# Kernel tuning notes

Hardware: AMD Instinct MI355X
Metric: run time of the kernel (lower is better)

The kernel has to match this reference:

```python
import jax, jax.numpy as jnp
import numpy as np

EMBED = 512
MLP_DIM = 2048
B, T = 4, 4096
EPS = 1e-5


def setup_inputs() -> dict:
    key = jax.random.key(0)
    ks = jax.random.split(key, 8)
    s = lambda fan_in: 1.0 / np.sqrt(fan_in)
    inp = {
        "x": jax.random.normal(ks[0], (B, T, EMBED), dtype=jnp.float32),
        "Wq": jax.random.uniform(ks[1], (EMBED, EMBED), jnp.float32, -s(EMBED), s(EMBED)),
        "bq": jnp.zeros((EMBED,), jnp.float32),
        "Wk": jax.random.uniform(ks[2], (EMBED, EMBED), jnp.float32, -s(EMBED), s(EMBED)),
        "bk": jnp.zeros((EMBED,), jnp.float32),
        "Wv": jax.random.uniform(ks[3], (EMBED, EMBED), jnp.float32, -s(EMBED), s(EMBED)),
        "bv": jnp.zeros((EMBED,), jnp.float32),
        "W1": jax.random.uniform(ks[4], (EMBED, MLP_DIM), jnp.float32, -s(EMBED), s(EMBED)),
        "b1": jnp.zeros((MLP_DIM,), jnp.float32),
        "W2": jax.random.uniform(ks[5], (MLP_DIM, EMBED), jnp.float32, -s(MLP_DIM), s(MLP_DIM)),
        "b2": jnp.zeros((EMBED,), jnp.float32),
        "ln1_g": jnp.ones((EMBED,), jnp.float32),
        "ln1_b": jnp.zeros((EMBED,), jnp.float32),
        "ln2_g": jnp.ones((EMBED,), jnp.float32),
        "ln2_b": jnp.zeros((EMBED,), jnp.float32),
    }
    return inp


def _layernorm(x, g, b):
    mu = x.mean(-1, keepdims=True)
    var = ((x - mu) ** 2).mean(-1, keepdims=True)
    return (x - mu) * jax.lax.rsqrt(var + EPS) * g + b


def reference(x, Wq, bq, Wk, bk, Wv, bv, W1, b1, W2, b2, ln1_g, ln1_b, ln2_g, ln2_b):
    # pre-LN causal self-attention (single head)
    h = _layernorm(x, ln1_g, ln1_b)
    q = h @ Wq + bq  # [B,T,D]
    k = h @ Wk + bk
    v = h @ Wv + bv
    scale = 1.0 / jnp.sqrt(jnp.float32(EMBED))
    scores = jnp.einsum("btd,bsd->bts", q, k) * scale  # [B,T,T]
    mask = jnp.tril(jnp.ones((T, T), dtype=bool))
    scores = jnp.where(mask, scores, -jnp.inf)
    # NOTE: source applies softmax over the ENTIRE [T,T] matrix per batch
    # element (global max + global sum), not per-row. Replicate exactly.
    m = scores.max(axis=(-2, -1), keepdims=True)
    e = jnp.exp(scores - m)
    attn = e / e.sum(axis=(-2, -1), keepdims=True)
    x = x + jnp.einsum("bts,bsd->btd", attn, v)
    # MLP
    h2 = _layernorm(x, ln2_g, ln2_b)
    x = x + (jax.nn.gelu(h2 @ W1 + b1, approximate=False) @ W2 + b2)
    return x
```

## Files before the change

### kernel.cpp

```cpp
#include <hip/hip_runtime.h>
#include <hip/hip_bf16.h>
#include <math.h>

#define EMBED 512
#define MLPD  2048
#define NB    4
#define TS    4096
#define BT    (NB*TS)
#define BK    64
#define NTILES_TRI 528

typedef __attribute__((ext_vector_type(4))) float f32x4;
typedef __attribute__((ext_vector_type(8))) short s16x8;
typedef __hip_bfloat16 bf16_t;

__device__ __forceinline__ void gload16(const void* g, void* l) {
  __builtin_amdgcn_global_load_lds(
      (const __attribute__((address_space(1))) void*)g,
      (__attribute__((address_space(3))) void*)l, 16, 0, 0);
}

__device__ __forceinline__ float fast_erf(float y) {
  const float ay = fabsf(y);
  const float t = __builtin_amdgcn_rcpf(1.0f + 0.3275911f*ay);
  float poly = 1.061405429f;
  poly = poly*t - 1.453152027f;
  poly = poly*t + 1.421413741f;
  poly = poly*t - 0.284496736f;
  poly = poly*t + 0.254829592f;
  poly = poly*t;
  const float e = 1.0f - poly*__expf(-ay*ay);
  return copysignf(e, y);
}


__device__ __forceinline__ void gemm_core(
    const bf16_t* __restrict__ A, int lda,
    const bf16_t* __restrict__ Bt, int ldb,
    int kmax, bf16_t* Alds, bf16_t* Blds, f32x4 acc[4][4])
{
  const int tid = threadIdx.x;
  const int w  = tid >> 6;
  const int l  = tid & 63;
  const int wr = w >> 1, wc = w & 1;
  const int fr = l & 15, fg = l >> 4;

  #pragma unroll
  for (int i = 0; i < 4; ++i)
    #pragma unroll
    for (int j = 0; j < 4; ++j)
      #pragma unroll
      for (int e = 0; e < 4; ++e)
        acc[i][j][e] = 0.0f;

  const int srow = w*32 + (l >> 3);
  const int sx = (((l & 7) ^ ((l >> 3) & 7)))*8;
  const int rsw = fr & 7;

  for (int k0 = 0; k0 < kmax; k0 += BK) {
    __syncthreads();
    #pragma unroll
    for (int c = 0; c < 4; ++c) {
      const bf16_t* ga = A  + (size_t)(srow + c*8)*lda + (k0 + sx);
      const bf16_t* gb = Bt + (size_t)(srow + c*8)*ldb + (k0 + sx);
      gload16(ga, Alds + (w*32 + c*8)*BK);
      gload16(gb, Blds + (w*32 + c*8)*BK);
    }
    __syncthreads();
    #pragma unroll
    for (int kk = 0; kk < BK; kk += 32) {
      s16x8 av[4], bv[4];
      const int ch = (kk >> 3) + fg;
      const int co = (ch ^ rsw) << 3;
      #pragma unroll
      for (int mf = 0; mf < 4; ++mf)
        av[mf] = *(const s16x8*)(Alds + (wr*64 + mf*16 + fr)*BK + co);
      #pragma unroll
      for (int nf = 0; nf < 4; ++nf)
        bv[nf] = *(const s16x8*)(Blds + (wc*64 + nf*16 + fr)*BK + co);
      #pragma unroll
      for (int mf = 0; mf < 4; ++mf)
        #pragma unroll
        for (int nf = 0; nf < 4; ++nf)
          acc[mf][nf] = __builtin_amdgcn_mfma_f32_16x16x32_bf16(
              av[mf], bv[nf], acc[mf][nf], 0, 0, 0);
    }
  }
}

__device__ __forceinline__ void gemm_core_deep(
    const bf16_t* __restrict__ A, int lda,
    const bf16_t* __restrict__ Bt, int ldb,
    int kmax, bf16_t* Alds, bf16_t* Blds, f32x4 acc[4][4])
{
  const int tid = threadIdx.x;
  const int w  = tid >> 6;
  const int l  = tid & 63;
  const int wr = w >> 1, wc = w & 1;
  const int fr = l & 15, fg = l >> 4;

  #pragma unroll
  for (int i = 0; i < 4; ++i)
    #pragma unroll
    for (int j = 0; j < 4; ++j)
      #pragma unroll
      for (int e = 0; e < 4; ++e)
        acc[i][j][e] = 0.0f;

  const int srow = w*32 + (l >> 3);
  const int sx = (((l & 7) ^ ((l >> 3) & 7)))*8;
  const int rsw = fr & 7;
  const int T = kmax >> 6;

  #define ISSUE_A(t_) do { \
    bf16_t* dst = Alds + ((t_) % 3)*(128*BK); \
    const int k0_ = (t_)*BK; \
    _Pragma("unroll") \
    for (int c = 0; c < 4; ++c) \
      gload16(A + (size_t)(srow + c*8)*lda + (k0_ + sx), dst + (w*32 + c*8)*BK); \
  } while (0)
  #define ISSUE_B(t_) do { \
    bf16_t* dst = Blds + ((t_) & 1)*(128*BK); \
    const int k0_ = (t_)*BK; \
    _Pragma("unroll") \
    for (int c = 0; c < 4; ++c) \
      gload16(Bt + (size_t)(srow + c*8)*ldb + (k0_ + sx), dst + (w*32 + c*8)*BK); \
  } while (0)

  ISSUE_A(0); ISSUE_B(0);
  if (T > 1) ISSUE_A(1);

  for (int t = 0; t < T; ++t) {
    if (t <= T - 3) {
      ISSUE_B(t + 1); ISSUE_A(t + 2);
      asm volatile("s_waitcnt vmcnt(12)" ::: "memory");
    } else if (t == T - 2) {
      ISSUE_B(t + 1);
      asm volatile("s_waitcnt vmcnt(8)" ::: "memory");
    } else {
      asm volatile("s_waitcnt vmcnt(0)" ::: "memory");
    }
    __builtin_amdgcn_s_barrier();
    bf16_t* Ac = Alds + (t % 3)*(128*BK);
    bf16_t* Bc = Blds + (t & 1)*(128*BK);
    #pragma unroll
    for (int kk = 0; kk < BK; kk += 32) {
      s16x8 av[4], bv[4];
      const int ch = (kk >> 3) + fg;
      const int co = (ch ^ rsw) << 3;
      #pragma unroll
      for (int mf = 0; mf < 4; ++mf)
        av[mf] = *(const s16x8*)(Ac + (wr*64 + mf*16 + fr)*BK + co);
      #pragma unroll
      for (int nf = 0; nf < 4; ++nf)
        bv[nf] = *(const s16x8*)(Bc + (wc*64 + nf*16 + fr)*BK + co);
      #pragma unroll
      for (int mf = 0; mf < 4; ++mf)
        #pragma unroll
        for (int nf = 0; nf < 4; ++nf)
          acc[mf][nf] = __builtin_amdgcn_mfma_f32_16x16x32_bf16(
              av[mf], bv[nf], acc[mf][nf], 0, 0, 0);
    }
    __builtin_amdgcn_s_barrier();
  }
  #undef ISSUE_A
  #undef ISSUE_B
}

#define EPILOGUE_SETUP \
  const int l = threadIdx.x & 63; const int w = threadIdx.x >> 6; \
  const int wr = w >> 1, wc = w & 1, fr = l & 15, fg = l >> 4;

__global__ void __launch_bounds__(256) k_proj_qkv(
    const bf16_t* __restrict__ A,
    const bf16_t* __restrict__ wqt, const bf16_t* __restrict__ wkt,
    const bf16_t* __restrict__ wvt,
    const float* __restrict__ bq, const float* __restrict__ bk,
    const float* __restrict__ bv,
    bf16_t* __restrict__ qb, bf16_t* __restrict__ kb, bf16_t* __restrict__ vt)
{
  __shared__ __align__(16) bf16_t Alds[128*BK];
  __shared__ __align__(16) bf16_t Blds[128*BK];
  f32x4 acc[4][4];
  const int z = blockIdx.z;
  const bf16_t* Wt = (z == 0) ? wqt : (z == 1) ? wkt : wvt;
  const float* bias = (z == 0) ? bq : (z == 1) ? bk : bv;
  const int bx = blockIdx.x;
  const int m0 = ((bx & 7)*16 + (bx >> 3))*128;
  const int n0 = blockIdx.y*128;
  gemm_core(A + (size_t)m0*EMBED, EMBED, Wt + (size_t)n0*EMBED, EMBED, EMBED,
            Alds, Blds, acc);
  EPILOGUE_SETUP
  if (z < 2) {
    bf16_t* outp = (z == 0) ? qb : kb;
    #pragma unroll
    for (int mf = 0; mf < 4; ++mf)
      #pragma unroll
      for (int nf = 0; nf < 4; ++nf) {
        const int col = n0 + wc*64 + nf*16 + fr;
        const float bb = bias[col];
        #pragma unroll
        for (int j = 0; j < 4; ++j) {
          const int row = m0 + wr*64 + mf*16 + fg*4 + j;
          outp[(size_t)row*EMBED + col] = __float2bfloat16(acc[mf][nf][j] + bb);
        }
      }
  } else {
    #pragma unroll
    for (int mf = 0; mf < 4; ++mf)
      #pragma unroll
      for (int nf = 0; nf < 4; ++nf) {
        const int col = n0 + wc*64 + nf*16 + fr;
        const float bb = bias[col];
        #pragma unroll
        for (int j = 0; j < 4; ++j) {
          const int row = m0 + wr*64 + mf*16 + fg*4 + j;
          const int b = row >> 12, t = row & 4095;
          vt[((size_t)b*EMBED + col)*TS + t] = __float2bfloat16(acc[mf][nf][j] + bb);
        }
      }
  }
}

__global__ void __launch_bounds__(256) k_attn1(
    const bf16_t* __restrict__ q, const bf16_t* __restrict__ kmat,
    bf16_t* __restrict__ P, float* __restrict__ partials, int serial_b)
{
  __shared__ __align__(16) bf16_t LB[2][128*BK];
  bf16_t* Alds = LB[0];
  bf16_t* Blds = LB[1];
  bf16_t* Plds = &LB[0][0];
  int b, r;
  if (serial_b >= 0) {
    b = serial_b; r = blockIdx.x;
  } else {
    const int L = blockIdx.x;
    const int logical = (L & 7)*264 + (L >> 3);
    b = logical / NTILES_TRI;
    r = logical - b*NTILES_TRI;
  }
  int ti = (int)((sqrtf(8.0f*(float)r + 1.0f) - 1.0f)*0.5f);
  while ((ti + 1)*(ti + 2)/2 <= r) ++ti;
  while (ti*(ti + 1)/2 > r) --ti;
  const int tj = r - ti*(ti + 1)/2;

  f32x4 acc[4][4];
  const bf16_t* A  = q    + ((size_t)b*TS + (size_t)ti*128)*EMBED;
  const bf16_t* Bt = kmat + ((size_t)b*TS + (size_t)tj*128)*EMBED;
  gemm_core(A, EMBED, Bt, EMBED, EMBED, Alds, Blds, acc);

  EPILOGUE_SETUP
  __syncthreads();
  const float SC = 0.044194173824159216f;
  float lsum = 0.0f;
  #pragma unroll
  for (int mf = 0; mf < 4; ++mf)
    #pragma unroll
    for (int nf = 0; nf < 4; ++nf) {
      const int ls = wc*64 + nf*16 + fr;
      const int gs = tj*128 + ls;
      const int chs = ((ls >> 3) ^ ((wr*64 + mf*16 + fg*4) & 7));
      (void)chs;
      #pragma unroll
      for (int j = 0; j < 4; ++j) {
        const int lt = wr*64 + mf*16 + fg*4 + j;
        const int gt = ti*128 + lt;
        float e = 0.0f;
        if (gs <= gt) e = __expf(acc[mf][nf][j]*SC - 30.0f);
        const int sc = (((ls >> 3) ^ (lt & 7)) << 3) | (ls & 7);
        Plds[lt*128 + sc] = __float2bfloat16(e);
        lsum += e;
      }
    }
  __syncthreads();
  bf16_t* Pb = P + (size_t)((serial_b >= 0) ? 0 : b)*TS*TS
                 + (size_t)ti*128*TS + tj*128;
  #pragma unroll
  for (int it = 0; it < 8; ++it) {
    const int row = w*32 + it*4 + (l >> 4);
    const int ch  = l & 15;
    const int chs2 = (ch & 8) | ((ch ^ (row & 7)) & 7);
    const s16x8 v = *(const s16x8*)(Plds + row*128 + chs2*8);
    *(s16x8*)(Pb + (size_t)row*TS + ch*8) = v;
  }
  #pragma unroll
  for (int off = 32; off > 0; off >>= 1) lsum += __shfl_xor(lsum, off);
  __shared__ float red[4];
  if (l == 0) red[w] = lsum;
  __syncthreads();
  if (threadIdx.x == 0)
    partials[(size_t)b*NTILES_TRI + r] = red[0] + red[1] + red[2] + red[3];
}

__global__ void k_reduce(const float* __restrict__ part, float* __restrict__ S, int n)
{
  const int b = blockIdx.x;
  const int l = threadIdx.x;
  float s = 0.0f;
  for (int i = l; i < n; i += 64) s += part[(size_t)b*n + i];
  #pragma unroll
  for (int off = 32; off > 0; off >>= 1) s += __shfl_xor(s, off);
  if (l == 0) S[b] = s;
}

__global__ void __launch_bounds__(256) k_attn2(
    const bf16_t* __restrict__ P, const bf16_t* __restrict__ vt,
    const float* __restrict__ S, const float* __restrict__ x,
    float* __restrict__ out, int serial_b)
{
  __shared__ __align__(16) bf16_t Alds[3*128*BK];
  __shared__ __align__(16) bf16_t Blds[2*128*BK];
  int ti, nj, b;
  if (serial_b >= 0) {
    ti = blockIdx.x; nj = blockIdx.y; b = serial_b;
  } else {
    const int L = blockIdx.x;
    const int xc = L & 7;
    const int idx = L >> 3;
    nj = idx & 3;
    const int s = idx >> 2;
    b = s & 3;
    const int which = s >> 2;
    ti = (which == 0) ? 2*xc
       : (which == 1) ? 2*xc + 1
       : (which == 2) ? 30 - 2*xc
                      : 31 - 2*xc;
  }
  f32x4 acc[4][4];
  const bf16_t* A  = P + (size_t)((serial_b >= 0) ? 0 : b)*TS*TS + (size_t)ti*128*TS;
  const bf16_t* Bt = vt + ((size_t)b*EMBED + (size_t)nj*128)*TS;
  const int kmax = (ti + 1)*128;
  gemm_core_deep(A, TS, Bt, TS, kmax, Alds, Blds, acc);

  EPILOGUE_SETUP
  const float invS = 1.0f / S[b];
  #pragma unroll
  for (int mf = 0; mf < 4; ++mf)
    #pragma unroll
    for (int nf = 0; nf < 4; ++nf) {
      const int d = nj*128 + wc*64 + nf*16 + fr;
      #pragma unroll
      for (int j = 0; j < 4; ++j) {
        const int t = ti*128 + wr*64 + mf*16 + fg*4 + j;
        const size_t idx2 = ((size_t)b*TS + t)*EMBED + d;
        out[idx2] = x[idx2] + acc[mf][nf][j]*invS;
      }
    }
}

__global__ void __launch_bounds__(256) k_mlp1(
    const bf16_t* __restrict__ A, const bf16_t* __restrict__ Wt,
    const float* __restrict__ bias, bf16_t* __restrict__ mid)
{
  __shared__ __align__(16) bf16_t Alds[128*BK];
  __shared__ __align__(16) bf16_t Blds[128*BK];
  f32x4 acc[4][4];
  const int L = blockIdx.x;
  const int xc = L & 7;
  const int i  = L >> 3;
  const int m0 = (xc*16 + (i & 15))*128;
  const int n0 = (i >> 4)*128;
  gemm_core(A + (size_t)m0*EMBED, EMBED, Wt + (size_t)n0*EMBED, EMBED, EMBED,
            Alds, Blds, acc);
  EPILOGUE_SETUP
  #pragma unroll
  for (int mf = 0; mf < 4; ++mf)
    #pragma unroll
    for (int nf = 0; nf < 4; ++nf) {
      const int col = n0 + wc*64 + nf*16 + fr;
      const float bb = bias[col];
      #pragma unroll
      for (int j = 0; j < 4; ++j) {
        const int row = m0 + wr*64 + mf*16 + fg*4 + j;
        const float pre = acc[mf][nf][j] + bb;
        const float ge = 0.5f*pre*(1.0f + fast_erf(pre*0.70710678118654752f));
        mid[(size_t)row*MLPD + col] = __float2bfloat16(ge);
      }
    }
}

__global__ void __launch_bounds__(256) k_mlp2(
    const bf16_t* __restrict__ A, const bf16_t* __restrict__ Wt,
    const float* __restrict__ bias, float* __restrict__ out)
{
  __shared__ __align__(16) bf16_t Alds[3*128*BK];
  __shared__ __align__(16) bf16_t Blds[2*128*BK];
  f32x4 acc[4][4];
  const int bx = blockIdx.x;
  const int m0 = ((bx & 7)*16 + (bx >> 3))*128;
  const int n0 = blockIdx.y*128;
  gemm_core_deep(A + (size_t)m0*MLPD, MLPD, Wt + (size_t)n0*MLPD, MLPD, MLPD,
                 Alds, Blds, acc);
  EPILOGUE_SETUP
  #pragma unroll
  for (int mf = 0; mf < 4; ++mf)
    #pragma unroll
    for (int nf = 0; nf < 4; ++nf) {
      const int col = n0 + wc*64 + nf*16 + fr;
      const float bb = bias[col];
      #pragma unroll
      for (int j = 0; j < 4; ++j) {
        const int row = m0 + wr*64 + mf*16 + fg*4 + j;
        const size_t idx = (size_t)row*EMBED + col;
        out[idx] = out[idx] + acc[mf][nf][j] + bb;
      }
    }
}

__global__ void __launch_bounds__(256) k_ln(
    const float* __restrict__ x, const float* __restrict__ g,
    const float* __restrict__ bta, bf16_t* __restrict__ h)
{
  const int row = blockIdx.x*4 + (threadIdx.x >> 6);
  const int l = threadIdx.x & 63;
  const float4* xr = (const float4*)(x + (size_t)row*EMBED);
  const float4 a = xr[l*2], c = xr[l*2 + 1];
  float vals[8] = {a.x, a.y, a.z, a.w, c.x, c.y, c.z, c.w};
  float s = 0.0f, ss = 0.0f;
  #pragma unroll
  for (int i = 0; i < 8; ++i) { s += vals[i]; ss += vals[i]*vals[i]; }
  #pragma unroll
  for (int off = 32; off > 0; off >>= 1) {
    s  += __shfl_xor(s,  off);
    ss += __shfl_xor(ss, off);
  }
  const float mu = s*(1.0f/EMBED);
  const float var = ss*(1.0f/EMBED) - mu*mu;
  const float rs = rsqrtf(var + 1e-5f);
  const float4* g4 = (const float4*)g;
  const float4* b4 = (const float4*)bta;
  const float4 ga = g4[l*2], gc = g4[l*2 + 1];
  const float4 ba = b4[l*2], bc = b4[l*2 + 1];
  const float gv[8] = {ga.x, ga.y, ga.z, ga.w, gc.x, gc.y, gc.z, gc.w};
  const float bv[8] = {ba.x, ba.y, ba.z, ba.w, bc.x, bc.y, bc.z, bc.w};
  s16x8 ov;
  bf16_t* ovp = (bf16_t*)&ov;
  #pragma unroll
  for (int i = 0; i < 8; ++i)
    ovp[i] = __float2bfloat16((vals[i] - mu)*rs*gv[i] + bv[i]);
  *((s16x8*)(h + (size_t)row*EMBED) + l) = ov;
}

__global__ void __launch_bounds__(256) k_transpose_all(
    const float* __restrict__ Wq, const float* __restrict__ Wk,
    const float* __restrict__ Wv, const float* __restrict__ W1,
    const float* __restrict__ W2,
    bf16_t* __restrict__ wqt, bf16_t* __restrict__ wkt,
    bf16_t* __restrict__ wvt, bf16_t* __restrict__ w1t,
    bf16_t* __restrict__ w2t)
{
  __shared__ float tile[32][33];
  int L = blockIdx.x;
  const float* W; bf16_t* Wt; int Kd, Nd, t;
  if (L < 768) {
    const int m = L >> 8; t = L & 255;
    W  = (m == 0) ? Wq : (m == 1) ? Wk : Wv;
    Wt = (m == 0) ? wqt : (m == 1) ? wkt : wvt;
    Kd = EMBED; Nd = EMBED;
  } else if (L < 1792) {
    t = L - 768;  W = W1; Wt = w1t; Kd = EMBED; Nd = MLPD;
  } else {
    t = L - 1792; W = W2; Wt = w2t; Kd = MLPD; Nd = EMBED;
  }
  const int ntx = Nd >> 5;
  const int tx32 = (t % ntx)*32, ty32 = (t / ntx)*32;
  const int x = threadIdx.x & 31, y8 = threadIdx.x >> 5;
  #pragma unroll
  for (int r = 0; r < 4; ++r) {
    const int y = y8 + r*8;
    tile[y][x] = W[(size_t)(ty32 + y)*Nd + tx32 + x];
  }
  __syncthreads();
  #pragma unroll
  for (int r = 0; r < 4; ++r) {
    const int y = y8 + r*8;
    Wt[(size_t)(tx32 + y)*Kd + ty32 + x] = __float2bfloat16(tile[x][y]);
  }
}

extern "C" void kernel_launch(void* const* d_in, const int* in_sizes, int n_in,
                              void* d_out, int out_size, void* d_ws, size_t ws_size,
                              hipStream_t stream) {
  (void)in_sizes; (void)n_in; (void)out_size;
  const float* x   = (const float*)d_in[0];
  const float* Wq  = (const float*)d_in[1];
  const float* bq  = (const float*)d_in[2];
  const float* Wk  = (const float*)d_in[3];
  const float* bk  = (const float*)d_in[4];
  const float* Wv  = (const float*)d_in[5];
  const float* bv  = (const float*)d_in[6];
  const float* W1  = (const float*)d_in[7];
  const float* b1  = (const float*)d_in[8];
  const float* W2  = (const float*)d_in[9];
  const float* b2  = (const float*)d_in[10];
  const float* g1  = (const float*)d_in[11];
  const float* be1 = (const float*)d_in[12];
  const float* g2  = (const float*)d_in[13];
  const float* be2 = (const float*)d_in[14];
  float* out = (float*)d_out;

  char* p = (char*)d_ws;
  auto alloc = [&](size_t bytes) -> char* {
    char* r = p; p += (bytes + 255) & ~(size_t)255; return r;
  };
  bf16_t* h   = (bf16_t*)alloc((size_t)BT*EMBED*2);
  bf16_t* wqt = (bf16_t*)alloc((size_t)EMBED*EMBED*2);
  bf16_t* wkt = (bf16_t*)alloc((size_t)EMBED*EMBED*2);
  bf16_t* wvt = (bf16_t*)alloc((size_t)EMBED*EMBED*2);
  bf16_t* w1t = (bf16_t*)alloc((size_t)MLPD*EMBED*2);
  bf16_t* w2t = (bf16_t*)alloc((size_t)EMBED*MLPD*2);
  bf16_t* qb  = (bf16_t*)alloc((size_t)BT*EMBED*2);
  bf16_t* kb  = (bf16_t*)alloc((size_t)BT*EMBED*2);
  bf16_t* vtb = (bf16_t*)alloc((size_t)BT*EMBED*2);
  float* partials = (float*)alloc((size_t)NB*NTILES_TRI*sizeof(float));
  float* S = (float*)alloc(256);

  const size_t mid_bytes = (size_t)BT*MLPD*2;
  const size_t p_full    = (size_t)NB*TS*TS*2;
  const size_t used = (size_t)(p - (char*)d_ws);
  const bool full = ws_size >= used + (p_full > mid_bytes ? p_full : mid_bytes);
  char* region = alloc(full ? p_full : mid_bytes);
  bf16_t* P   = (bf16_t*)region;
  bf16_t* mid = (bf16_t*)region;

  k_transpose_all<<<dim3(2816), 256, 0, stream>>>(Wq, Wk, Wv, W1, W2,
                                                  wqt, wkt, wvt, w1t, w2t);
  k_ln<<<BT/4, 256, 0, stream>>>(x, g1, be1, h);

  k_proj_qkv<<<dim3(BT/128, EMBED/128, 3), 256, 0, stream>>>(
      h, wqt, wkt, wvt, bq, bk, bv, qb, kb, vtb);

  if (full) {
    k_attn1<<<dim3(NB*NTILES_TRI), 256, 0, stream>>>(qb, kb, P, partials, -1);
    k_reduce<<<NB, 64, 0, stream>>>(partials, S, NTILES_TRI);
    k_attn2<<<dim3(512), 256, 0, stream>>>(P, vtb, S, x, out, -1);
  } else {
    for (int b = 0; b < NB; ++b) {
      k_attn1<<<dim3(NTILES_TRI), 256, 0, stream>>>(qb, kb, P, partials, b);
      k_reduce<<<1, 64, 0, stream>>>(partials + (size_t)b*NTILES_TRI, S + b, NTILES_TRI);
      k_attn2<<<dim3(TS/128, EMBED/128), 256, 0, stream>>>(P, vtb, S, x, out, b);
    }
  }

  k_ln<<<BT/4, 256, 0, stream>>>(out, g2, be2, h);
  k_mlp1<<<dim3(2048), 256, 0, stream>>>(h, w1t, b1, mid);
  k_mlp2<<<dim3(BT/128, EMBED/128), 256, 0, stream>>>(mid, w2t, b2, out);
}
```

Baseline: 301.1 us.

## Stage MLP1 output through LDS for coalesced stores; use deep pipeline; drop tile swizzle

The MLP1 epilogue now writes GELU results into a swizzled LDS tile and then stores them to global memory as 16-byte vectors per row, replacing scattered 2-byte stores. MLP1 also switches to the deeper-buffered gemm core and a 2D grid. The XCD-aware block remapping is removed from the QKV, MLP1 and MLP2 kernels in favour of plain row-major block indices. The price is extra LDS use and two barriers in MLP1, plus possibly worse L2 locality once the remapping is gone.

```diff
diff --git a/kernel.cpp b/kernel.cpp
--- a/kernel.cpp
+++ b/kernel.cpp
@@ -185,9 +185,7 @@
   const int z = blockIdx.z;
   const bf16_t* Wt = (z == 0) ? wqt : (z == 1) ? wkt : wvt;
   const float* bias = (z == 0) ? bq : (z == 1) ? bk : bv;
-  const int bx = blockIdx.x;
-  const int m0 = ((bx & 7)*16 + (bx >> 3))*128;
-  const int n0 = blockIdx.y*128;
+  const int m0 = blockIdx.x*128, n0 = blockIdx.y*128;
   gemm_core(A + (size_t)m0*EMBED, EMBED, Wt + (size_t)n0*EMBED, EMBED, EMBED,
             Alds, Blds, acc);
   EPILOGUE_SETUP
@@ -259,8 +257,6 @@
     for (int nf = 0; nf < 4; ++nf) {
       const int ls = wc*64 + nf*16 + fr;
       const int gs = tj*128 + ls;
-      const int chs = ((ls >> 3) ^ ((wr*64 + mf*16 + fg*4) & 7));
-      (void)chs;
       #pragma unroll
       for (int j = 0; j < 4; ++j) {
         const int lt = wr*64 + mf*16 + fg*4 + j;
@@ -352,31 +348,40 @@
     const bf16_t* __restrict__ A, const bf16_t* __restrict__ Wt,
     const float* __restrict__ bias, bf16_t* __restrict__ mid)
 {
-  __shared__ __align__(16) bf16_t Alds[128*BK];
-  __shared__ __align__(16) bf16_t Blds[128*BK];
+  __shared__ __align__(16) bf16_t Alds[3*128*BK];
+  __shared__ __align__(16) bf16_t Blds[2*128*BK];
   f32x4 acc[4][4];
-  const int L = blockIdx.x;
-  const int xc = L & 7;
-  const int i  = L >> 3;
-  const int m0 = (xc*16 + (i & 15))*128;
-  const int n0 = (i >> 4)*128;
-  gemm_core(A + (size_t)m0*EMBED, EMBED, Wt + (size_t)n0*EMBED, EMBED, EMBED,
-            Alds, Blds, acc);
+  const int m0 = blockIdx.x*128, n0 = blockIdx.y*128;
+  gemm_core_deep(A + (size_t)m0*EMBED, EMBED, Wt + (size_t)n0*EMBED, EMBED, EMBED,
+                 Alds, Blds, acc);
   EPILOGUE_SETUP
+  bf16_t* Plds = Alds;
+  __syncthreads();
   #pragma unroll
   for (int mf = 0; mf < 4; ++mf)
     #pragma unroll
     for (int nf = 0; nf < 4; ++nf) {
-      const int col = n0 + wc*64 + nf*16 + fr;
-      const float bb = bias[col];
+      const int ls = wc*64 + nf*16 + fr;
+      const float bb = bias[n0 + ls];
       #pragma unroll
       for (int j = 0; j < 4; ++j) {
-        const int row = m0 + wr*64 + mf*16 + fg*4 + j;
+        const int lt = wr*64 + mf*16 + fg*4 + j;
         const float pre = acc[mf][nf][j] + bb;
         const float ge = 0.5f*pre*(1.0f + fast_erf(pre*0.70710678118654752f));
-        mid[(size_t)row*MLPD + col] = __float2bfloat16(ge);
+        const int sc = (((ls >> 3) ^ (lt & 7)) << 3) | (ls & 7);
+        Plds[lt*128 + sc] = __float2bfloat16(ge);
       }
     }
+  __syncthreads();
+  bf16_t* Mb = mid + (size_t)m0*MLPD + n0;
+  #pragma unroll
+  for (int it = 0; it < 8; ++it) {
+    const int row = w*32 + it*4 + (l >> 4);
+    const int ch  = l & 15;
+    const int chs2 = (ch & 8) | ((ch ^ (row & 7)) & 7);
+    const s16x8 v = *(const s16x8*)(Plds + row*128 + chs2*8);
+    *(s16x8*)(Mb + (size_t)row*MLPD + ch*8) = v;
+  }
 }
 
 __global__ void __launch_bounds__(256) k_mlp2(
@@ -386,9 +391,7 @@
   __shared__ __align__(16) bf16_t Alds[3*128*BK];
   __shared__ __align__(16) bf16_t Blds[2*128*BK];
   f32x4 acc[4][4];
-  const int bx = blockIdx.x;
-  const int m0 = ((bx & 7)*16 + (bx >> 3))*128;
-  const int n0 = blockIdx.y*128;
+  const int m0 = blockIdx.x*128, n0 = blockIdx.y*128;
   gemm_core_deep(A + (size_t)m0*MLPD, MLPD, Wt + (size_t)n0*MLPD, MLPD, MLPD,
                  Alds, Blds, acc);
   EPILOGUE_SETUP
@@ -543,6 +546,6 @@
   }
 
   k_ln<<<BT/4, 256, 0, stream>>>(out, g2, be2, h);
-  k_mlp1<<<dim3(2048), 256, 0, stream>>>(h, w1t, b1, mid);
+  k_mlp1<<<dim3(BT/128, MLPD/128), 256, 0, stream>>>(h, w1t, b1, mid);
   k_mlp2<<<dim3(BT/128, EMBED/128), 256, 0, stream>>>(mid, w2t, b2, out);
 }
```

New measurement: 329.0 us. 9.3% more time.
